# Kernel optimization log

Hardware: AMD Instinct MI355X
Metric: run time of the kernel (lower is better)

The kernel has to match this reference:

```python
import jax, jax.numpy as jnp
import numpy as np
from jax.scipy.special import erf

B, N, D = 4, 4096, 2
MU, ALPHA, BETA, SIGMA = 1.0, 0.8, 2.0, 0.02


def setup_inputs() -> dict:
    key = jax.random.key(0)
    k1, k2 = jax.random.split(key)
    locations = jax.random.uniform(k1, (B, N, D), dtype=jnp.float32)  # events in unit box
    times = jnp.sort(jax.random.uniform(k2, (B, N), dtype=jnp.float32), axis=-1)  # sorted event times
    # ragged sequence lengths via mask
    lengths = jnp.array([N, N - 256, N - 512, N - 1024], dtype=jnp.int32)
    mask = jnp.arange(N)[None, :] < lengths[:, None]
    return {
        "locations": locations,
        "times": times,
        "mask": mask,
        "mu": jnp.float32(MU),
        "alpha": jnp.float32(ALPHA),
        "beta": jnp.float32(BETA),
        "sigma": jnp.float32(SIGMA),
        "spatial_low": jnp.zeros((D,), jnp.float32),
        "spatial_high": jnp.ones((D,), jnp.float32),
        "t_end": jnp.float32(1.0),
    }


def reference(locations, times, mask, mu, alpha, beta, sigma, spatial_low, spatial_high, t_end):
    """Hawkes log_prob: sum_i log lambda*(s_i, t_i | H_{t_i}) - Lambda(D x [0, T])."""
    d = locations.shape[-1]
    # --- intensity at each event given its (strictly earlier, masked) history ---
    dt = times[:, :, None] - times[:, None, :]            # [B,N,N] t_i - t_j
    valid = (dt > 0.0) & mask[:, None, :]                 # causal + observed history
    dt_safe = jnp.where(valid, dt, 0.0)
    diff = locations[:, :, None, :] - locations[:, None, :, :]  # [B,N,N,D]
    sqdist = jnp.sum(diff * diff, axis=-1)                # [B,N,N]
    two_sig2 = 2.0 * sigma * sigma
    # fused exp of temporal decay * spatial Gaussian exponent
    kern = jnp.where(valid, jnp.exp(-beta * dt_safe - sqdist / two_sig2), 0.0)
    norm = beta / (jnp.pi * two_sig2) ** (d / 2)          # beta * (2*pi*sigma^2)^(-d/2)
    lam = mu + alpha * norm * jnp.sum(kern, axis=-1)      # [B,N]
    log_lam = jnp.sum(jnp.where(mask, jnp.log(lam), 0.0), axis=-1)  # [B]
    # --- compensator with erf boundary correction ---
    s_sqrt2 = sigma * jnp.sqrt(jnp.float32(2.0))
    cdf = 0.5 * (erf((spatial_high - locations) / s_sqrt2)
                 - erf((spatial_low - locations) / s_sqrt2))        # [B,N,D]
    in_domain_mass = jnp.prod(cdf, axis=-1)               # [B,N]
    temporal_mass = 1.0 - jnp.exp(-beta * (t_end - times))  # [B,N]
    area = jnp.prod(spatial_high - spatial_low)
    comp = mu * area * t_end + alpha * jnp.sum(
        jnp.where(mask, temporal_mass * in_domain_mass, 0.0), axis=-1)  # [B]
    return log_lam - comp
```

## Files before the change

kernel.cpp:

```cpp
#include <hip/hip_runtime.h>
#include <math.h>

#define NB   4096
#define BB   4
#define TI   256
#define TJ   128
#define NSL  (NB / TJ)
#define THR  128
#define TPB  272

#if __has_builtin(__builtin_amdgcn_exp2f)
#define EXP2F __builtin_amdgcn_exp2f
#else
#define EXP2F exp2f
#endif

#define S_ELEMS (BB * NSL * NB)

__global__ __launch_bounds__(THR) void hawkes_pair(
    const float* __restrict__ loc, const float* __restrict__ times,
    const int* __restrict__ mask,
    const float* __restrict__ beta_p, const float* __restrict__ sigma_p,
    float* __restrict__ S)
{
    const int b  = blockIdx.x / TPB;
    const int k  = blockIdx.x % TPB;
    int it = (int)floorf((sqrtf((float)(4 * k + 1)) - 1.0f) * 0.5f);
    while ((it + 1) * (it + 1) + (it + 1) <= k) ++it;
    while (it * it + it > k) --it;
    const int s = k - (it * it + it);

    const int tid = threadIdx.x;

    if (k == 0 && tid == 0) {
        float* acc = S + S_ELEMS;
        acc[b] = 0.0f;
        acc[BB + b] = 0.0f;
        ((int*)(acc + 2 * BB))[b] = 0;
    }

    const int i0 = it * TI + tid;
    const int i1 = i0 + THR;

    const float beta  = beta_p[0];
    const float sigma = sigma_p[0];
    const float L2E = 1.4426950408889634f;
    const float nb  = -beta * L2E;
    const float nc  = -L2E / (2.0f * sigma * sigma);

    const float t0 = times[b * NB + i0];
    const float x0 = loc[(b * NB + i0) * 2 + 0];
    const float y0 = loc[(b * NB + i0) * 2 + 1];
    const float u0 = fmaf(nc, fmaf(x0, x0, y0 * y0), nb * t0);
    const float t1 = times[b * NB + i1];
    const float x1 = loc[(b * NB + i1) * 2 + 0];
    const float y1 = loc[(b * NB + i1) * 2 + 1];
    const float u1 = fmaf(nc, fmaf(x1, x1, y1 * y1), nb * t1);

    __shared__ float4 jt[TJ];
    {
        const int j  = s * TJ + tid;
        const float tj = times[b * NB + j];
        const float xj = loc[(b * NB + j) * 2 + 0];
        const float yj = loc[(b * NB + j) * 2 + 1];
        const bool  mj = mask[b * NB + j] != 0;
        float4 v;
        v.x = mj ? fmaf(nc, fmaf(xj, xj, yj * yj), -nb * tj) : -3.0e38f;
        v.y = mj ? (-2.0f * nc * xj) : 0.0f;
        v.z = mj ? (-2.0f * nc * yj) : 0.0f;
        v.w = mj ? tj : 2.0f;
        jt[tid] = v;
    }
    __syncthreads();

    float a0 = 0.0f, a1 = 0.0f;
    if (s < 2 * it) {
#pragma unroll 8
        for (int jj = 0; jj < TJ; ++jj) {
            float4 v = jt[jj];
            float g0 = fmaf(v.y, x0, fmaf(v.z, y0, u0 + v.x));
            float g1 = fmaf(v.y, x1, fmaf(v.z, y1, u1 + v.x));
            a0 += EXP2F(g0);
            a1 += EXP2F(g1);
        }
    } else {
#pragma unroll 8
        for (int jj = 0; jj < TJ; ++jj) {
            float4 v = jt[jj];
            float g0 = fmaf(v.y, x0, fmaf(v.z, y0, u0 + v.x));
            float g1 = fmaf(v.y, x1, fmaf(v.z, y1, u1 + v.x));
            float e0 = EXP2F(g0);
            float e1 = EXP2F(g1);
            a0 += (t0 > v.w) ? e0 : 0.0f;
            a1 += (t1 > v.w) ? e1 : 0.0f;
        }
    }
    float* __restrict__ Srow = S + (size_t)(b * NSL + s) * NB;
    Srow[i0] = a0;
    Srow[i1] = a1;
}

__global__ __launch_bounds__(256) void hawkes_finish(
    const float* __restrict__ loc, const float* __restrict__ times,
    const int* __restrict__ mask,
    const float* mu_p, const float* alpha_p, const float* beta_p, const float* sigma_p,
    const float* lo_p, const float* hi_p, const float* tend_p,
    float* __restrict__ S, float* __restrict__ out)
{
    const int b   = blockIdx.x >> 4;
    const int r   = blockIdx.x & 15;
    const int tid = threadIdx.x;
    const int i   = r * 256 + tid;

    const float mu    = mu_p[0];
    const float alpha = alpha_p[0];
    const float beta  = beta_p[0];
    const float sigma = sigma_p[0];
    const float lo0 = lo_p[0], lo1 = lo_p[1];
    const float hi0 = hi_p[0], hi1 = hi_p[1];
    const float tend = tend_p[0];

    const float two_sig2 = 2.0f * sigma * sigma;
    const float an = alpha * beta / ((float)M_PI * two_sig2);
    const float inv_ss2 = 1.0f / (sigma * sqrtf(2.0f));

    float accL = 0.0f, accC = 0.0f;
    if (mask[b * NB + i] != 0) {
        const int smax = 2 * (i >> 8) + 2;
        float sum = 0.0f;
        for (int s = 0; s < smax; ++s)
            sum += S[(size_t)(b * NSL + s) * NB + i];
        float lam = fmaf(an, sum, mu);
        accL = logf(lam);
        float tmass = 1.0f - expf(-beta * (tend - times[b * NB + i]));
        float x = loc[(b * NB + i) * 2 + 0];
        float y = loc[(b * NB + i) * 2 + 1];
        float cx = 0.5f * (erff((hi0 - x) * inv_ss2) - erff((lo0 - x) * inv_ss2));
        float cy = 0.5f * (erff((hi1 - y) * inv_ss2) - erff((lo1 - y) * inv_ss2));
        accC = tmass * cx * cy;
    }

    __shared__ float redL[4], redC[4];
    for (int off = 32; off > 0; off >>= 1) {
        accL += __shfl_down(accL, off, 64);
        accC += __shfl_down(accC, off, 64);
    }
    const int wave = tid >> 6, lane = tid & 63;
    if (lane == 0) { redL[wave] = accL; redC[wave] = accC; }
    __syncthreads();

    if (tid == 0) {
        float L = redL[0] + redL[1] + redL[2] + redL[3];
        float C = redC[0] + redC[1] + redC[2] + redC[3];
        float* accLg = S + S_ELEMS;
        float* accCg = accLg + BB;
        int*   cnt   = (int*)(accLg + 2 * BB);
        atomicAdd(&accLg[b], L);
        atomicAdd(&accCg[b], C);
        __threadfence();
        int old = atomicAdd(&cnt[b], 1);
        if (old == 15) {
            __threadfence();
            float Lt = atomicAdd(&accLg[b], 0.0f);
            float Ct = atomicAdd(&accCg[b], 0.0f);
            float area = (hi0 - lo0) * (hi1 - lo1);
            out[b] = Lt - (mu * area * tend + alpha * Ct);
        }
    }
}

extern "C" void kernel_launch(void* const* d_in, const int* in_sizes, int n_in,
                              void* d_out, int out_size, void* d_ws, size_t ws_size,
                              hipStream_t stream) {
    const float* loc   = (const float*)d_in[0];
    const float* times = (const float*)d_in[1];
    const int*   mask  = (const int*)d_in[2];
    const float* mu_p    = (const float*)d_in[3];
    const float* alpha_p = (const float*)d_in[4];
    const float* beta_p  = (const float*)d_in[5];
    const float* sigma_p = (const float*)d_in[6];
    const float* lo_p    = (const float*)d_in[7];
    const float* hi_p    = (const float*)d_in[8];
    const float* tend_p  = (const float*)d_in[9];
    float* out = (float*)d_out;
    float* S   = (float*)d_ws;

    hawkes_pair<<<dim3(BB * TPB), THR, 0, stream>>>(loc, times, mask, beta_p, sigma_p, S);
    hawkes_finish<<<dim3(BB * 16), 256, 0, stream>>>(loc, times, mask, mu_p, alpha_p, beta_p,
                                                     sigma_p, lo_p, hi_p, tend_p, S, out);
}
```

Baseline: 92.33 us.

## Fuse pair and finish kernels into one cooperative launch with grid sync

Merges the pairwise-sum kernel and the reduction/finish kernel into a single cooperative kernel that uses a grid-wide barrier in place of a second launch. The first 32 blocks per batch then do the finish work with 128 threads each. This is meant to remove the launch gap between the two kernels. In exchange it adds the cost of a grid sync and the overhead of a cooperative launch, and it requires all 1088 blocks to be co-resident.

```diff
diff --git a/kernel.cpp b/kernel.cpp
--- a/kernel.cpp
+++ b/kernel.cpp
@@ -1,5 +1,8 @@
 #include <hip/hip_runtime.h>
+#include <hip/hip_cooperative_groups.h>
 #include <math.h>
+
+namespace cg = cooperative_groups;
 
 #define NB   4096
 #define BB   4
@@ -8,6 +11,7 @@
 #define NSL  (NB / TJ)
 #define THR  128
 #define TPB  272
+#define NFIN (NB / THR)
 
 #if __has_builtin(__builtin_amdgcn_exp2f)
 #define EXP2F __builtin_amdgcn_exp2f
@@ -17,11 +21,13 @@
 
 #define S_ELEMS (BB * NSL * NB)
 
-__global__ __launch_bounds__(THR) void hawkes_pair(
+__global__ __launch_bounds__(THR) void hawkes_coop(
     const float* __restrict__ loc, const float* __restrict__ times,
     const int* __restrict__ mask,
-    const float* __restrict__ beta_p, const float* __restrict__ sigma_p,
-    float* __restrict__ S)
+    const float* mu_p, const float* alpha_p,
+    const float* beta_p, const float* sigma_p,
+    const float* lo_p, const float* hi_p, const float* tend_p,
+    float* __restrict__ S, float* __restrict__ out)
 {
     const int b  = blockIdx.x / TPB;
     const int k  = blockIdx.x % TPB;
@@ -39,23 +45,23 @@
         ((int*)(acc + 2 * BB))[b] = 0;
     }
 
-    const int i0 = it * TI + tid;
-    const int i1 = i0 + THR;
-
     const float beta  = beta_p[0];
     const float sigma = sigma_p[0];
     const float L2E = 1.4426950408889634f;
-    const float nb  = -beta * L2E;
+    const float nbt = -beta * L2E;
     const float nc  = -L2E / (2.0f * sigma * sigma);
+
+    const int i0 = it * TI + tid;
+    const int i1 = i0 + THR;
 
     const float t0 = times[b * NB + i0];
     const float x0 = loc[(b * NB + i0) * 2 + 0];
     const float y0 = loc[(b * NB + i0) * 2 + 1];
-    const float u0 = fmaf(nc, fmaf(x0, x0, y0 * y0), nb * t0);
+    const float u0 = fmaf(nc, fmaf(x0, x0, y0 * y0), nbt * t0);
     const float t1 = times[b * NB + i1];
     const float x1 = loc[(b * NB + i1) * 2 + 0];
     const float y1 = loc[(b * NB + i1) * 2 + 1];
-    const float u1 = fmaf(nc, fmaf(x1, x1, y1 * y1), nb * t1);
+    const float u1 = fmaf(nc, fmaf(x1, x1, y1 * y1), nbt * t1);
 
     __shared__ float4 jt[TJ];
     {
@@ -65,7 +71,7 @@
         const float yj = loc[(b * NB + j) * 2 + 1];
         const bool  mj = mask[b * NB + j] != 0;
         float4 v;
-        v.x = mj ? fmaf(nc, fmaf(xj, xj, yj * yj), -nb * tj) : -3.0e38f;
+        v.x = mj ? fmaf(nc, fmaf(xj, xj, yj * yj), -nbt * tj) : -3.0e38f;
         v.y = mj ? (-2.0f * nc * xj) : 0.0f;
         v.z = mj ? (-2.0f * nc * yj) : 0.0f;
         v.w = mj ? tj : 2.0f;
@@ -98,24 +104,15 @@
     float* __restrict__ Srow = S + (size_t)(b * NSL + s) * NB;
     Srow[i0] = a0;
     Srow[i1] = a1;
-}
 
-__global__ __launch_bounds__(256) void hawkes_finish(
-    const float* __restrict__ loc, const float* __restrict__ times,
-    const int* __restrict__ mask,
-    const float* mu_p, const float* alpha_p, const float* beta_p, const float* sigma_p,
-    const float* lo_p, const float* hi_p, const float* tend_p,
-    float* __restrict__ S, float* __restrict__ out)
-{
-    const int b   = blockIdx.x >> 4;
-    const int r   = blockIdx.x & 15;
-    const int tid = threadIdx.x;
-    const int i   = r * 256 + tid;
+    __threadfence();
+    cg::this_grid().sync();
 
+    if (k >= NFIN) return;
+
+    const int i = k * THR + tid;
     const float mu    = mu_p[0];
     const float alpha = alpha_p[0];
-    const float beta  = beta_p[0];
-    const float sigma = sigma_p[0];
     const float lo0 = lo_p[0], lo1 = lo_p[1];
     const float hi0 = hi_p[0], hi1 = hi_p[1];
     const float tend = tend_p[0];
@@ -128,8 +125,8 @@
     if (mask[b * NB + i] != 0) {
         const int smax = 2 * (i >> 8) + 2;
         float sum = 0.0f;
-        for (int s = 0; s < smax; ++s)
-            sum += S[(size_t)(b * NSL + s) * NB + i];
+        for (int q = 0; q < smax; ++q)
+            sum += S[(size_t)(b * NSL + q) * NB + i];
         float lam = fmaf(an, sum, mu);
         accL = logf(lam);
         float tmass = 1.0f - expf(-beta * (tend - times[b * NB + i]));
@@ -140,18 +137,18 @@
         accC = tmass * cx * cy;
     }
 
-    __shared__ float redL[4], redC[4];
     for (int off = 32; off > 0; off >>= 1) {
         accL += __shfl_down(accL, off, 64);
         accC += __shfl_down(accC, off, 64);
     }
+    __shared__ float redL[2], redC[2];
     const int wave = tid >> 6, lane = tid & 63;
     if (lane == 0) { redL[wave] = accL; redC[wave] = accC; }
     __syncthreads();
 
     if (tid == 0) {
-        float L = redL[0] + redL[1] + redL[2] + redL[3];
-        float C = redC[0] + redC[1] + redC[2] + redC[3];
+        float L = redL[0] + redL[1];
+        float C = redC[0] + redC[1];
         float* accLg = S + S_ELEMS;
         float* accCg = accLg + BB;
         int*   cnt   = (int*)(accLg + 2 * BB);
@@ -159,7 +156,7 @@
         atomicAdd(&accCg[b], C);
         __threadfence();
         int old = atomicAdd(&cnt[b], 1);
-        if (old == 15) {
+        if (old == NFIN - 1) {
             __threadfence();
             float Lt = atomicAdd(&accLg[b], 0.0f);
             float Ct = atomicAdd(&accCg[b], 0.0f);
@@ -185,7 +182,12 @@
     float* out = (float*)d_out;
     float* S   = (float*)d_ws;
 
-    hawkes_pair<<<dim3(BB * TPB), THR, 0, stream>>>(loc, times, mask, beta_p, sigma_p, S);
-    hawkes_finish<<<dim3(BB * 16), 256, 0, stream>>>(loc, times, mask, mu_p, alpha_p, beta_p,
-                                                     sigma_p, lo_p, hi_p, tend_p, S, out);
+    void* args[] = {
+        (void*)&loc, (void*)&times, (void*)&mask,
+        (void*)&mu_p, (void*)&alpha_p, (void*)&beta_p, (void*)&sigma_p,
+        (void*)&lo_p, (void*)&hi_p, (void*)&tend_p,
+        (void*)&S, (void*)&out
+    };
+    hipLaunchCooperativeKernel((const void*)hawkes_coop,
+                               dim3(BB * TPB), dim3(THR), args, 0, stream);
 }
```

After: 186.4 us. +101.9%, slower.
